# Optimization experiments

Hardware: AMD Instinct MI355X
Metric: run time of the kernel (lower is better)

Reference implementation:

```python
import jax, jax.numpy as jnp
import numpy as np

B, C, H, W = 4, 64, 64, 64

def setup_inputs() -> dict:
    key = jax.random.key(0)
    ks = jax.random.split(key, 9)
    return {
        "x": jax.random.normal(ks[0], (B, C, H, W), dtype=jnp.float32),
        "Wq": jax.random.normal(ks[1], (C, C), dtype=jnp.float32) * (1.0 / np.sqrt(C)),
        "bq": jax.random.normal(ks[2], (C,), dtype=jnp.float32) * 0.02,
        "Wk": jax.random.normal(ks[3], (C, C), dtype=jnp.float32) * (1.0 / np.sqrt(C)),
        "bk": jax.random.normal(ks[4], (C,), dtype=jnp.float32) * 0.02,
        "Wv": jax.random.normal(ks[5], (C, C), dtype=jnp.float32) * (1.0 / np.sqrt(C)),
        "bv": jax.random.normal(ks[6], (C,), dtype=jnp.float32) * 0.02,
        "rel_h": jax.random.normal(ks[7], (1, C, H, 1), dtype=jnp.float32),
        "rel_w": jax.random.normal(ks[8], (1, C, 1, W), dtype=jnp.float32),
    }

def reference(x, Wq, bq, Wk, bk, Wv, bv, rel_h, rel_w):
    b, c, h, w = x.shape
    n = h * w
    xf = x.reshape(b, c, n)                                  # [B,C,N]
    # 1x1 convs == channel-wise linear maps (weight [out,in])
    q = jnp.einsum('oc,bcn->bno', Wq, xf) + bq               # [B,N,C]
    k = jnp.einsum('oc,bcn->bon', Wk, xf) + bk[:, None]      # [B,C,N]
    v = jnp.einsum('oc,bcn->bon', Wv, xf) + bv[:, None]      # [B,C,N]
    energy = jnp.einsum('bnc,bcm->bnm', q, k)                # content term [B,N,N]
    pos = (rel_h + rel_w).reshape(c, n)                      # [C,N]
    energy = energy + jnp.einsum('bnc,cm->bnm', q, pos)      # add positional bias
    attn = jax.nn.softmax(energy, axis=-1)                   # [B,N,N]
    # out[b,c,n] = sum_m v[b,c,m] * attn[b,n,m]  (bmm with attention^T)
    out = jnp.einsum('bcm,bnm->bcn', v, attn)
    return out.reshape(b, c, h, w)
```

## Files before the change

kernel.cpp:

```cpp
#include <hip/hip_runtime.h>
#include <math.h>

#define NPOS 4096
#define NB   4
#define NROW (NB * NPOS)
#define LOG2E 1.44269504088896f

typedef _Float16 f16;
typedef f16 f16x4 __attribute__((ext_vector_type(4)));
typedef f16 f16x8 __attribute__((ext_vector_type(8)));
typedef float f32x4 __attribute__((ext_vector_type(4)));

#define LDW 72

__global__ __launch_bounds__(256) void qkv_proj(
    const float* __restrict__ x,
    const float* __restrict__ Wq, const float* __restrict__ bq,
    const float* __restrict__ Wk, const float* __restrict__ bk,
    const float* __restrict__ Wv, const float* __restrict__ bv,
    const float* __restrict__ rel_h, const float* __restrict__ rel_w,
    f16* __restrict__ qh, f16* __restrict__ kh, f16* __restrict__ vh)
{
    __shared__ __align__(16) f16 Ws[192 * LDW];
    __shared__ __align__(16) f16 Xs[16 * LDW];
    __shared__ __align__(16) f16 Vs[64 * 20];

    const int tid = threadIdx.x;
    const int b   = blockIdx.x >> 8;
    const int n0  = (blockIdx.x & 255) << 4;

    #pragma unroll
    for (int k = 0; k < 12; ++k) {
        int idx  = tid + k * 256;
        int orow = idx >> 4;
        int cseg = (idx & 15) << 2;
        int mat  = orow >> 6;
        int o    = orow & 63;
        const float* wsrc = (mat == 0) ? Wq : ((mat == 1) ? Wk : Wv);
        float4 v = *(const float4*)(wsrc + o * 64 + cseg);
        f16x4 h; h[0] = (f16)v.x; h[1] = (f16)v.y; h[2] = (f16)v.z; h[3] = (f16)v.w;
        *(f16x4*)(&Ws[orow * LDW + cseg]) = h;
    }
    {
        int c  = tid >> 2;
        int ns = (tid & 3) << 2;
        float4 v = *(const float4*)(x + ((size_t)(b * 64 + c)) * NPOS + n0 + ns);
        Xs[(ns + 0) * LDW + c] = (f16)v.x;
        Xs[(ns + 1) * LDW + c] = (f16)v.y;
        Xs[(ns + 2) * LDW + c] = (f16)v.z;
        Xs[(ns + 3) * LDW + c] = (f16)v.w;
    }
    __syncthreads();

    const int wave = tid >> 6;
    const int lane = tid & 63;
    const int quad = lane >> 4;
    const int l16  = lane & 15;

    const f16x8 a0 = *(const f16x8*)(&Xs[l16 * LDW + quad * 8]);
    const f16x8 a1 = *(const f16x8*)(&Xs[l16 * LDW + 32 + quad * 8]);

    f32x4 acc[3];
    const int t0 = wave * 3;
    #pragma unroll
    for (int i = 0; i < 3; ++i) {
        int t = t0 + i;
        f32x4 c0 = {0, 0, 0, 0};
        f16x8 b0 = *(const f16x8*)(&Ws[(t * 16 + l16) * LDW + quad * 8]);
        f16x8 b1 = *(const f16x8*)(&Ws[(t * 16 + l16) * LDW + 32 + quad * 8]);
        c0 = __builtin_amdgcn_mfma_f32_16x16x32_f16(a0, b0, c0, 0, 0, 0);
        c0 = __builtin_amdgcn_mfma_f32_16x16x32_f16(a1, b1, c0, 0, 0, 0);
        acc[i] = c0;
    }

    #pragma unroll
    for (int i = 0; i < 3; ++i) {
        int t = t0 + i;
        if (t < 4) {
            int o = t * 16 + l16;
            float bb = bq[o];
            #pragma unroll
            for (int r = 0; r < 4; ++r) {
                size_t n = (size_t)b * NPOS + n0 + quad * 4 + r;
                qh[n * 64 + o] = (f16)((acc[i][r] + bb) * LOG2E);
            }
        } else if (t < 8) {
            int o = (t - 4) * 16 + l16;
            int h = n0 >> 6;
            int wbase = n0 & 63;
            float bb = bk[o] + rel_h[o * 64 + h];
            #pragma unroll
            for (int r = 0; r < 4; ++r) {
                size_t n = (size_t)b * NPOS + n0 + quad * 4 + r;
                kh[n * 64 + o] = (f16)(acc[i][r] + bb + rel_w[o * 64 + wbase + quad * 4 + r]);
            }
        } else {
            int o = (t - 8) * 16 + l16;
            float bb = bv[o];
            #pragma unroll
            for (int r = 0; r < 4; ++r)
                Vs[o * 20 + quad * 4 + r] = (f16)(acc[i][r] + bb);
        }
    }
    __syncthreads();
    {
        int c  = tid >> 2;
        int ns = (tid & 3) << 2;
        f16x4 vv = *(const f16x4*)(&Vs[c * 20 + ns]);
        *(f16x4*)(vh + ((size_t)(b * 64 + c)) * NPOS + n0 + ns) = vv;
    }
}

#define LDP 72

__global__ __launch_bounds__(256, 8) void attn(
    const f16* __restrict__ qh, const f16* __restrict__ kh,
    const f16* __restrict__ vh,
    f16* __restrict__ Op, float* __restrict__ Mp, float* __restrict__ Lp,
    int split, int mchunk)
{
    __shared__ __align__(16) f16 Ks[64 * LDP];
    __shared__ __align__(16) f16 Vt[64 * LDP];

    const int tid  = threadIdx.x;
    const int wave = tid >> 6;
    const int lane = tid & 63;
    const int quad = lane >> 4;
    const int l16  = lane & 15;
    const int s    = blockIdx.x % split;
    const int tile = blockIdx.x / split;
    const int b    = tile >> 6;
    const int n0   = (tile & 63) << 6;

    const f16* qbase = qh + ((size_t)b * NPOS + n0 + wave * 16 + l16) * 64;
    const f16x8 bq0 = *(const f16x8*)(qbase + quad * 8);
    const f16x8 bq1 = *(const f16x8*)(qbase + 32 + quad * 8);

    f32x4 O[4] = {{0,0,0,0},{0,0,0,0},{0,0,0,0},{0,0,0,0}};
    float m_i = -1e30f, l_i = 0.f;

    const int srow = tid >> 2;
    const int sseg = (tid & 3) * 16;
    const f16* kb = kh + (size_t)b * NPOS * 64;
    const f16* vb = vh + (size_t)b * 64 * NPOS;

    const int m_begin = s * mchunk;
    for (int m0 = m_begin; m0 < m_begin + mchunk; m0 += 64) {
        const f16* ksrc = kb + (size_t)(m0 + srow) * 64 + sseg;
        *(f16x8*)(&Ks[srow * LDP + sseg])     = *(const f16x8*)(ksrc);
        *(f16x8*)(&Ks[srow * LDP + sseg + 8]) = *(const f16x8*)(ksrc + 8);
        const f16* vsrc = vb + (size_t)srow * NPOS + m0 + sseg;
        *(f16x8*)(&Vt[srow * LDP + sseg])     = *(const f16x8*)(vsrc);
        *(f16x8*)(&Vt[srow * LDP + sseg + 8]) = *(const f16x8*)(vsrc + 8);
        __syncthreads();

        f32x4 S[4];
        #pragma unroll
        for (int t = 0; t < 4; ++t) {
            f32x4 acc = {0, 0, 0, 0};
            f16x8 ak0 = *(const f16x8*)(&Ks[(t * 16 + l16) * LDP + quad * 8]);
            f16x8 ak1 = *(const f16x8*)(&Ks[(t * 16 + l16) * LDP + 32 + quad * 8]);
            acc = __builtin_amdgcn_mfma_f32_16x16x32_f16(ak0, bq0, acc, 0, 0, 0);
            acc = __builtin_amdgcn_mfma_f32_16x16x32_f16(ak1, bq1, acc, 0, 0, 0);
            S[t] = acc;
        }

        float mx = S[0][0];
        #pragma unroll
        for (int t = 0; t < 4; ++t)
            #pragma unroll
            for (int r = 0; r < 4; ++r) mx = fmaxf(mx, S[t][r]);
        mx = fmaxf(mx, __shfl_xor(mx, 16));
        mx = fmaxf(mx, __shfl_xor(mx, 32));

        if (__any(mx > m_i)) {
            float mnew  = fmaxf(m_i, mx);
            float alpha = __builtin_amdgcn_exp2f(m_i - mnew);
            m_i = mnew;
            l_i *= alpha;
            #pragma unroll
            for (int r = 0; r < 4; ++r) {
                float av = __shfl(alpha, quad * 20 + r);
                O[0][r] *= av; O[1][r] *= av; O[2][r] *= av; O[3][r] *= av;
            }
        }

        float rs = 0.f;
        f16x4 pa[4];
        #pragma unroll
        for (int t = 0; t < 4; ++t) {
            f16x4 a;
            #pragma unroll
            for (int r = 0; r < 4; ++r) {
                float e = __builtin_amdgcn_exp2f(S[t][r] - m_i);
                rs += e;
                a[r] = (f16)e;
            }
            pa[t] = a;
        }
        rs += __shfl_xor(rs, 16);
        rs += __shfl_xor(rs, 32);
        l_i += rs;

        #pragma unroll
        for (int u = 0; u < 4; ++u) {
            #pragma unroll
            for (int t = 0; t < 4; ++t) {
                f16x4 bf = *(const f16x4*)(&Vt[(u * 16 + l16) * LDP + t * 16 + quad * 4]);
                O[u] = __builtin_amdgcn_mfma_f32_16x16x16f16(pa[t], bf, O[u], 0, 0, 0);
            }
        }
        __syncthreads();
    }

    #pragma unroll
    for (int r = 0; r < 4; ++r) {
        float lr  = __shfl(l_i, quad * 20 + r);
        float inv = 1.f / lr;
        size_t row = (size_t)b * NPOS + n0 + wave * 16 + quad * 4 + r;
        #pragma unroll
        for (int u = 0; u < 4; ++u)
            Op[((size_t)s * NROW + row) * 64 + u * 16 + l16] = (f16)(O[u][r] * inv);
    }
    if (lane < 16) {
        size_t row = (size_t)b * NPOS + n0 + wave * 16 + l16;
        Mp[(size_t)s * NROW + row] = m_i;
        Lp[(size_t)s * NROW + row] = l_i;
    }
}

__global__ __launch_bounds__(256) void combine(
    const f16* __restrict__ Op, const float* __restrict__ Mp,
    const float* __restrict__ Lp, float* __restrict__ out, int split)
{
    __shared__ float Ot[16 * 68];

    const int tid = threadIdx.x;
    const int b   = blockIdx.x >> 8;
    const int n0  = (blockIdx.x & 255) << 4;

    {
        int nl = tid >> 4;
        int cs = (tid & 15) << 2;
        size_t row = (size_t)b * NPOS + n0 + nl;

        float M = -1e30f;
        for (int s2 = 0; s2 < split; ++s2)
            M = fmaxf(M, Mp[(size_t)s2 * NROW + row]);

        float L = 0.f;
        float val[4] = {0.f, 0.f, 0.f, 0.f};
        for (int s2 = 0; s2 < split; ++s2) {
            float w = Lp[(size_t)s2 * NROW + row] *
                      __builtin_amdgcn_exp2f(Mp[(size_t)s2 * NROW + row] - M);
            L += w;
            f16x4 o0 = *(const f16x4*)(Op + ((size_t)s2 * NROW + row) * 64 + cs);
            #pragma unroll
            for (int j = 0; j < 4; ++j) val[j] += w * (float)o0[j];
        }
        float invL = 1.f / L;
        float4 v4 = { val[0] * invL, val[1] * invL, val[2] * invL, val[3] * invL };
        *(float4*)(&Ot[nl * 68 + cs]) = v4;
    }
    __syncthreads();
    {
        int c  = tid >> 2;
        int ns = (tid & 3) << 2;
        float4 v4 = { Ot[(ns + 0) * 68 + c], Ot[(ns + 1) * 68 + c],
                      Ot[(ns + 2) * 68 + c], Ot[(ns + 3) * 68 + c] };
        *(float4*)(out + ((size_t)(b * 64 + c)) * NPOS + n0 + ns) = v4;
    }
}

extern "C" void kernel_launch(void* const* d_in, const int* in_sizes, int n_in,
                              void* d_out, int out_size, void* d_ws, size_t ws_size,
                              hipStream_t stream) {
    const float* x     = (const float*)d_in[0];
    const float* Wq    = (const float*)d_in[1];
    const float* bq    = (const float*)d_in[2];
    const float* Wk    = (const float*)d_in[3];
    const float* bk    = (const float*)d_in[4];
    const float* Wv    = (const float*)d_in[5];
    const float* bv    = (const float*)d_in[6];
    const float* rel_h = (const float*)d_in[7];
    const float* rel_w = (const float*)d_in[8];
    float* out = (float*)d_out;

    const size_t qkv_elems = (size_t)NROW * 64;
    int split = 8;
    {
        size_t need = 3 * qkv_elems * sizeof(f16)
                    + (size_t)split * NROW * 64 * sizeof(f16)
                    + 2 * (size_t)split * NROW * sizeof(float);
        if (ws_size < need) split = 4;
    }
    const int mchunk = NPOS / split;

    f16* qh = (f16*)d_ws;
    f16* kh = qh + qkv_elems;
    f16* vh = kh + qkv_elems;
    f16* Op = vh + qkv_elems;
    float* Mp = (float*)(Op + (size_t)split * NROW * 64);
    float* Lp = Mp + (size_t)split * NROW;

    qkv_proj<<<NB * (NPOS / 16), 256, 0, stream>>>(x, Wq, bq, Wk, bk, Wv, bv,
                                                   rel_h, rel_w, qh, kh, vh);
    attn<<<NB * (NPOS / 64) * split, 256, 0, stream>>>(qh, kh, vh, Op, Mp, Lp,
                                                       split, mchunk);
    combine<<<NB * (NPOS / 16), 256, 0, stream>>>(Op, Mp, Lp, out, split);
}
```

Before: 127.4 us.

## Load K fragments directly from global and double-buffer V tile in LDS

The attention kernel no longer stages K in shared memory: each wave reads its K fragments straight from global memory into registers for the QK MFMA. V is now double-buffered in LDS, with the next tile prefetched while the current one is consumed, leaving one barrier per iteration instead of two. This trades LDS traffic and a sync for redundant global/L2 reads of K across the four waves, and LDS use stays roughly the same.

```diff
diff --git a/kernel.cpp b/kernel.cpp
--- a/kernel.cpp
+++ b/kernel.cpp
@@ -111,7 +111,7 @@
     }
 }
 
-#define LDP 72
+#define LDV 72
 
 __global__ __launch_bounds__(256, 8) void attn(
     const f16* __restrict__ qh, const f16* __restrict__ kh,
@@ -119,8 +119,7 @@
     f16* __restrict__ Op, float* __restrict__ Mp, float* __restrict__ Lp,
     int split, int mchunk)
 {
-    __shared__ __align__(16) f16 Ks[64 * LDP];
-    __shared__ __align__(16) f16 Vt[64 * LDP];
+    __shared__ __align__(16) f16 Vt[2][64 * LDV];
 
     const int tid  = threadIdx.x;
     const int wave = tid >> 6;
@@ -139,27 +138,36 @@
     f32x4 O[4] = {{0,0,0,0},{0,0,0,0},{0,0,0,0},{0,0,0,0}};
     float m_i = -1e30f, l_i = 0.f;
 
-    const int srow = tid >> 2;
-    const int sseg = (tid & 3) * 16;
+    const int vrow = tid >> 2;
+    const int vseg = (tid & 3) * 16;
     const f16* kb = kh + (size_t)b * NPOS * 64;
     const f16* vb = vh + (size_t)b * 64 * NPOS;
 
     const int m_begin = s * mchunk;
-    for (int m0 = m_begin; m0 < m_begin + mchunk; m0 += 64) {
-        const f16* ksrc = kb + (size_t)(m0 + srow) * 64 + sseg;
-        *(f16x8*)(&Ks[srow * LDP + sseg])     = *(const f16x8*)(ksrc);
-        *(f16x8*)(&Ks[srow * LDP + sseg + 8]) = *(const f16x8*)(ksrc + 8);
-        const f16* vsrc = vb + (size_t)srow * NPOS + m0 + sseg;
-        *(f16x8*)(&Vt[srow * LDP + sseg])     = *(const f16x8*)(vsrc);
-        *(f16x8*)(&Vt[srow * LDP + sseg + 8]) = *(const f16x8*)(vsrc + 8);
-        __syncthreads();
+    const int m_end   = m_begin + mchunk;
+
+    {
+        const f16* vsrc = vb + (size_t)vrow * NPOS + m_begin + vseg;
+        *(f16x8*)(&Vt[0][vrow * LDV + vseg])     = *(const f16x8*)(vsrc);
+        *(f16x8*)(&Vt[0][vrow * LDV + vseg + 8]) = *(const f16x8*)(vsrc + 8);
+    }
+    __syncthreads();
+
+    int buf = 0;
+    for (int m0 = m_begin; m0 < m_end; m0 += 64) {
+        if (m0 + 64 < m_end) {
+            const f16* vsrc = vb + (size_t)vrow * NPOS + (m0 + 64) + vseg;
+            *(f16x8*)(&Vt[buf ^ 1][vrow * LDV + vseg])     = *(const f16x8*)(vsrc);
+            *(f16x8*)(&Vt[buf ^ 1][vrow * LDV + vseg + 8]) = *(const f16x8*)(vsrc + 8);
+        }
 
         f32x4 S[4];
         #pragma unroll
         for (int t = 0; t < 4; ++t) {
+            const f16* krow = kb + (size_t)(m0 + t * 16 + l16) * 64;
+            f16x8 ak0 = *(const f16x8*)(krow + quad * 8);
+            f16x8 ak1 = *(const f16x8*)(krow + 32 + quad * 8);
             f32x4 acc = {0, 0, 0, 0};
-            f16x8 ak0 = *(const f16x8*)(&Ks[(t * 16 + l16) * LDP + quad * 8]);
-            f16x8 ak1 = *(const f16x8*)(&Ks[(t * 16 + l16) * LDP + 32 + quad * 8]);
             acc = __builtin_amdgcn_mfma_f32_16x16x32_f16(ak0, bq0, acc, 0, 0, 0);
             acc = __builtin_amdgcn_mfma_f32_16x16x32_f16(ak1, bq1, acc, 0, 0, 0);
             S[t] = acc;
@@ -206,11 +214,12 @@
         for (int u = 0; u < 4; ++u) {
             #pragma unroll
             for (int t = 0; t < 4; ++t) {
-                f16x4 bf = *(const f16x4*)(&Vt[(u * 16 + l16) * LDP + t * 16 + quad * 4]);
+                f16x4 bf = *(const f16x4*)(&Vt[buf][(u * 16 + l16) * LDV + t * 16 + quad * 4]);
                 O[u] = __builtin_amdgcn_mfma_f32_16x16x16f16(pa[t], bf, O[u], 0, 0, 0);
             }
         }
         __syncthreads();
+        buf ^= 1;
     }
 
     #pragma unroll
```

Measured after the change: 153.7 us. 20.6% more time.

## Process two query row groups per wave to reuse K/V tiles

Applied to the files above, without the earlier changes.

Each attention block now covers 128 query rows instead of 64, with every wave handling two 16-row groups. This lets the K and V shared-memory tiles and their LDS fragment reads be reused across twice as many MFMAs, halving global K/V loads per query. The costs are doubled accumulator register use (occupancy hint lowered from 8 to 4), half as many blocks in the grid, and the same split-K partitioning as before.

```diff
diff --git a/kernel.cpp b/kernel.cpp
--- a/kernel.cpp
+++ b/kernel.cpp
@@ -113,7 +113,7 @@
 
 #define LDP 72
 
-__global__ __launch_bounds__(256, 8) void attn(
+__global__ __launch_bounds__(256, 4) void attn(
     const f16* __restrict__ qh, const f16* __restrict__ kh,
     const f16* __restrict__ vh,
     f16* __restrict__ Op, float* __restrict__ Mp, float* __restrict__ Lp,
@@ -129,15 +129,20 @@
     const int l16  = lane & 15;
     const int s    = blockIdx.x % split;
     const int tile = blockIdx.x / split;
-    const int b    = tile >> 6;
-    const int n0   = (tile & 63) << 6;
-
-    const f16* qbase = qh + ((size_t)b * NPOS + n0 + wave * 16 + l16) * 64;
-    const f16x8 bq0 = *(const f16x8*)(qbase + quad * 8);
-    const f16x8 bq1 = *(const f16x8*)(qbase + 32 + quad * 8);
-
-    f32x4 O[4] = {{0,0,0,0},{0,0,0,0},{0,0,0,0},{0,0,0,0}};
-    float m_i = -1e30f, l_i = 0.f;
+    const int b    = tile >> 5;
+    const int n0   = (tile & 31) << 7;
+
+    f16x8 bq0[2], bq1[2];
+    #pragma unroll
+    for (int g = 0; g < 2; ++g) {
+        const f16* qbase = qh + ((size_t)b * NPOS + n0 + wave * 32 + g * 16 + l16) * 64;
+        bq0[g] = *(const f16x8*)(qbase + quad * 8);
+        bq1[g] = *(const f16x8*)(qbase + 32 + quad * 8);
+    }
+
+    f32x4 O[2][4] = {{{0,0,0,0},{0,0,0,0},{0,0,0,0},{0,0,0,0}},
+                     {{0,0,0,0},{0,0,0,0},{0,0,0,0},{0,0,0,0}}};
+    float m_i[2] = {-1e30f, -1e30f}, l_i[2] = {0.f, 0.f};
 
     const int srow = tid >> 2;
     const int sseg = (tid & 3) * 16;
@@ -154,78 +159,89 @@
         *(f16x8*)(&Vt[srow * LDP + sseg + 8]) = *(const f16x8*)(vsrc + 8);
         __syncthreads();
 
-        f32x4 S[4];
+        f32x4 S[2][4];
         #pragma unroll
         for (int t = 0; t < 4; ++t) {
-            f32x4 acc = {0, 0, 0, 0};
             f16x8 ak0 = *(const f16x8*)(&Ks[(t * 16 + l16) * LDP + quad * 8]);
             f16x8 ak1 = *(const f16x8*)(&Ks[(t * 16 + l16) * LDP + 32 + quad * 8]);
-            acc = __builtin_amdgcn_mfma_f32_16x16x32_f16(ak0, bq0, acc, 0, 0, 0);
-            acc = __builtin_amdgcn_mfma_f32_16x16x32_f16(ak1, bq1, acc, 0, 0, 0);
-            S[t] = acc;
-        }
-
-        float mx = S[0][0];
+            #pragma unroll
+            for (int g = 0; g < 2; ++g) {
+                f32x4 acc = {0, 0, 0, 0};
+                acc = __builtin_amdgcn_mfma_f32_16x16x32_f16(ak0, bq0[g], acc, 0, 0, 0);
+                acc = __builtin_amdgcn_mfma_f32_16x16x32_f16(ak1, bq1[g], acc, 0, 0, 0);
+                S[g][t] = acc;
+            }
+        }
+
+        f16x4 pa[2][4];
         #pragma unroll
-        for (int t = 0; t < 4; ++t)
-            #pragma unroll
-            for (int r = 0; r < 4; ++r) mx = fmaxf(mx, S[t][r]);
-        mx = fmaxf(mx, __shfl_xor(mx, 16));
-        mx = fmaxf(mx, __shfl_xor(mx, 32));
-
-        if (__any(mx > m_i)) {
-            float mnew  = fmaxf(m_i, mx);
-            float alpha = __builtin_amdgcn_exp2f(m_i - mnew);
-            m_i = mnew;
-            l_i *= alpha;
-            #pragma unroll
-            for (int r = 0; r < 4; ++r) {
-                float av = __shfl(alpha, quad * 20 + r);
-                O[0][r] *= av; O[1][r] *= av; O[2][r] *= av; O[3][r] *= av;
-            }
-        }
-
-        float rs = 0.f;
-        f16x4 pa[4];
-        #pragma unroll
-        for (int t = 0; t < 4; ++t) {
-            f16x4 a;
-            #pragma unroll
-            for (int r = 0; r < 4; ++r) {
-                float e = __builtin_amdgcn_exp2f(S[t][r] - m_i);
-                rs += e;
-                a[r] = (f16)e;
-            }
-            pa[t] = a;
-        }
-        rs += __shfl_xor(rs, 16);
-        rs += __shfl_xor(rs, 32);
-        l_i += rs;
+        for (int g = 0; g < 2; ++g) {
+            float mx = S[g][0][0];
+            #pragma unroll
+            for (int t = 0; t < 4; ++t)
+                #pragma unroll
+                for (int r = 0; r < 4; ++r) mx = fmaxf(mx, S[g][t][r]);
+            mx = fmaxf(mx, __shfl_xor(mx, 16));
+            mx = fmaxf(mx, __shfl_xor(mx, 32));
+
+            if (__any(mx > m_i[g])) {
+                float mnew  = fmaxf(m_i[g], mx);
+                float alpha = __builtin_amdgcn_exp2f(m_i[g] - mnew);
+                m_i[g] = mnew;
+                l_i[g] *= alpha;
+                #pragma unroll
+                for (int r = 0; r < 4; ++r) {
+                    float av = __shfl(alpha, quad * 20 + r);
+                    O[g][0][r] *= av; O[g][1][r] *= av;
+                    O[g][2][r] *= av; O[g][3][r] *= av;
+                }
+            }
+
+            float rs = 0.f;
+            #pragma unroll
+            for (int t = 0; t < 4; ++t) {
+                f16x4 a;
+                #pragma unroll
+                for (int r = 0; r < 4; ++r) {
+                    float e = __builtin_amdgcn_exp2f(S[g][t][r] - m_i[g]);
+                    rs += e;
+                    a[r] = (f16)e;
+                }
+                pa[g][t] = a;
+            }
+            rs += __shfl_xor(rs, 16);
+            rs += __shfl_xor(rs, 32);
+            l_i[g] += rs;
+        }
 
         #pragma unroll
         for (int u = 0; u < 4; ++u) {
             #pragma unroll
             for (int t = 0; t < 4; ++t) {
                 f16x4 bf = *(const f16x4*)(&Vt[(u * 16 + l16) * LDP + t * 16 + quad * 4]);
-                O[u] = __builtin_amdgcn_mfma_f32_16x16x16f16(pa[t], bf, O[u], 0, 0, 0);
+                O[0][u] = __builtin_amdgcn_mfma_f32_16x16x16f16(pa[0][t], bf, O[0][u], 0, 0, 0);
+                O[1][u] = __builtin_amdgcn_mfma_f32_16x16x16f16(pa[1][t], bf, O[1][u], 0, 0, 0);
             }
         }
         __syncthreads();
     }
 
     #pragma unroll
-    for (int r = 0; r < 4; ++r) {
-        float lr  = __shfl(l_i, quad * 20 + r);
-        float inv = 1.f / lr;
-        size_t row = (size_t)b * NPOS + n0 + wave * 16 + quad * 4 + r;
+    for (int g = 0; g < 2; ++g) {
         #pragma unroll
-        for (int u = 0; u < 4; ++u)
-            Op[((size_t)s * NROW + row) * 64 + u * 16 + l16] = (f16)(O[u][r] * inv);
-    }
-    if (lane < 16) {
-        size_t row = (size_t)b * NPOS + n0 + wave * 16 + l16;
-        Mp[(size_t)s * NROW + row] = m_i;
-        Lp[(size_t)s * NROW + row] = l_i;
+        for (int r = 0; r < 4; ++r) {
+            float lr  = __shfl(l_i[g], quad * 20 + r);
+            float inv = 1.f / lr;
+            size_t row = (size_t)b * NPOS + n0 + wave * 32 + g * 16 + quad * 4 + r;
+            #pragma unroll
+            for (int u = 0; u < 4; ++u)
+                Op[((size_t)s * NROW + row) * 64 + u * 16 + l16] = (f16)(O[g][u][r] * inv);
+        }
+        if (lane < 16) {
+            size_t row = (size_t)b * NPOS + n0 + wave * 32 + g * 16 + l16;
+            Mp[(size_t)s * NROW + row] = m_i[g];
+            Lp[(size_t)s * NROW + row] = l_i[g];
+        }
     }
 }
 
@@ -305,7 +321,7 @@
 
     qkv_proj<<<NB * (NPOS / 16), 256, 0, stream>>>(x, Wq, bq, Wk, bk, Wv, bv,
                                                    rel_h, rel_w, qh, kh, vh);
-    attn<<<NB * (NPOS / 64) * split, 256, 0, stream>>>(qh, kh, vh, Op, Mp, Lp,
-                                                       split, mchunk);
+    attn<<<NB * (NPOS / 128) * split, 256, 0, stream>>>(qh, kh, vh, Op, Mp, Lp,
+                                                        split, mchunk);
     combine<<<NB * (NPOS / 16), 256, 0, stream>>>(Op, Mp, Lp, out, split);
 }
```

New measurement: 117.5 us. -7.7%, faster.
